# Performance work log

Measured on AMD Instinct MI355X. Metric: run time of the kernel, lower is better.

Reference implementation:

```python
import jax, jax.numpy as jnp
import numpy as np

SHAPE = (64, 64, 64)
N0 = 4000
K = 5  # subm conv kernel size -> 125 taps


def _neighbors(coors, shp):
    # coors: [N,4] int (b,z,y,x), batch=1. Returns [N,125] int32 neighbor row ids, -1 if absent.
    offs = np.stack(np.meshgrid(np.arange(-2, 3), np.arange(-2, 3), np.arange(-2, 3), indexing='ij'), -1).reshape(-1, 3)
    shp = np.asarray(shp)
    grid = -np.ones(tuple(shp), np.int32)
    grid[coors[:, 1], coors[:, 2], coors[:, 3]] = np.arange(len(coors), dtype=np.int32)
    nb = coors[:, None, 1:4] + offs[None]  # [N,125,3]
    valid = ((nb >= 0) & (nb < shp)).all(-1)
    nbc = np.clip(nb, 0, shp - 1)
    nbr = grid[nbc[..., 0], nbc[..., 1], nbc[..., 2]]
    return np.where(valid, nbr, -1).astype(np.int32)


def _pool_map(coors, shp):
    # kernel 2 stride 2 sparse max pool: parent cell = spatial // 2
    out_shp = [s // 2 for s in shp]
    sp = coors[:, 1:4] // 2
    lin = (sp[:, 0] * out_shp[1] + sp[:, 1]) * out_shp[2] + sp[:, 2]
    uniq, inv = np.unique(lin, return_inverse=True)
    z = uniq // (out_shp[1] * out_shp[2])
    r = uniq % (out_shp[1] * out_shp[2])
    nc = np.stack([np.zeros_like(z), z, r // out_shp[2], r % out_shp[2]], 1).astype(np.int32)
    return inv.astype(np.int32), nc, out_shp


_PAIRS = [(3, 64), (64, 64), (64, 96), (96, 96), (96, 128), (128, 128), (128, 160), (160, 160), (160, 192), (192, 192), (192, 224), (224, 224), (224, 256), (256, 256)]
_WNAMES = ['w0a', 'w0b', 'w1a', 'w1b', 'w2a', 'w2b', 'w3a', 'w3b', 'w4a', 'w4b', 'w5a', 'w5b', 'w6a', 'w6b']


def setup_inputs() -> dict:
    rng = np.random.RandomState(0)
    lin = rng.choice(SHAPE[0] * SHAPE[1] * SHAPE[2], N0, replace=False)
    z = lin // (SHAPE[1] * SHAPE[2])
    r = lin % (SHAPE[1] * SHAPE[2])
    coors = np.stack([np.zeros_like(z), z, r // SHAPE[2], r % SHAPE[2]], 1).astype(np.int32)
    inp = {}
    c, shp = coors, list(SHAPE)
    for l in range(7):
        inp['nbr%d' % l] = jnp.asarray(_neighbors(c, shp))
        if l < 6:
            pm, c, shp = _pool_map(c, shp)
            inp['pool%d' % l] = jnp.asarray(pm)
    key = jax.random.key(0)
    for name, (ci, co) in zip(_WNAMES, _PAIRS):
        key, k = jax.random.split(key)
        inp[name] = jax.random.normal(k, (K ** 3, ci, co), jnp.float32) * (K ** 3 * ci) ** -0.5
    key, kf = jax.random.split(key)
    inp['features'] = jax.random.normal(kf, (N0, 3), jnp.float32)
    inp['coors'] = jnp.asarray(coors)
    inp['batch_size'] = 1
    return inp


def _subm(feats, nbr, w):
    # gather-GEMM-scatter form of SubMConv3d (bias=False): out active set == in active set
    valid = nbr >= 0  # [N,125]
    g = jnp.take(feats, jnp.maximum(nbr, 0), axis=0)  # [N,125,Cin]
    g = jnp.where(valid[:, :, None], g, jnp.zeros((), feats.dtype))
    return jnp.einsum('nkc,kco->no', g, w)  # [N,Cout]


def reference(features, coors, batch_size, nbr0, nbr1, nbr2, nbr3, nbr4, nbr5, nbr6, pool0, pool1, pool2, pool3, pool4, pool5, w0a, w0b, w1a, w1b, w2a, w2b, w3a, w3b, w4a, w4b, w5a, w5b, w6a, w6b):
    nbrs = (nbr0, nbr1, nbr2, nbr3, nbr4, nbr5, nbr6)
    pools = (pool0, pool1, pool2, pool3, pool4, pool5)
    ws = ((w0a, w0b), (w1a, w1b), (w2a, w2b), (w3a, w3b), (w4a, w4b), (w5a, w5b), (w6a, w6b))
    x = features
    for l in range(7):
        x = _subm(x, nbrs[l], ws[l][0])
        x = _subm(x, nbrs[l], ws[l][1])
        if l < 6:
            # sparse max pool over active voxels of each 2x2x2 cell
            x = jax.ops.segment_max(x, pools[l], num_segments=nbrs[l + 1].shape[0])
    return x
```

## Files before the change

### kernel.cpp

```cpp
#include <hip/hip_runtime.h>
#include <stddef.h>
#include <stdint.h>

#define KTAPS 125

typedef _Float16 f16x8 __attribute__((ext_vector_type(8)));
typedef _Float16 f16x4 __attribute__((ext_vector_type(4)));
typedef float    f32x4 __attribute__((ext_vector_type(4)));

template<int NT>
__global__ __launch_bounds__(256) void subm_mfma(
    const _Float16* __restrict__ finh, const int* __restrict__ nbr,
    const _Float16* __restrict__ wt, _Float16* __restrict__ Pout,
    int N, int CinP, int TS)
{
    constexpr int BN = NT * 32;
    constexpr int DEPTH = (NT <= 5) ? 4 : 2;
    __shared__ int       nbs[16][64];
    __shared__ unsigned  msk[16][2];
    __shared__ unsigned char vtl[2][16];
    __shared__ int       vcs[2];
    __shared__ unsigned short sjc[2][128];

    const int tid  = threadIdx.x;
    const int lane = tid & 63;
    const int wid  = tid >> 6;
    const int wy   = wid & 1;
    const int wx   = wid >> 1;
    const int r15  = lane & 15;
    const int g4   = lane >> 4;
    const int row0 = blockIdx.x * 64;
    const int k0   = (blockIdx.y * KTAPS) / TS;
    const int k1   = ((blockIdx.y + 1) * KTAPS) / TS;
    const int KR   = k1 - k0;
    const int CC   = CinP >> 5;

    #pragma unroll
    for (int p = 0; p < 4; ++p) {
        int e = tid + p * 256;
        if (e < KR * 64) {
            int j = e >> 6, r = e & 63;
            int gr = row0 + r;
            nbs[j][r] = (gr < N) ? nbr[(size_t)gr * KTAPS + k0 + j] : -1;
        }
    }
    __syncthreads();
    for (int j = wid; j < KR; j += 4) {
        unsigned long long m = __ballot(nbs[j][lane] >= 0);
        if (lane == 0) { msk[j][0] = (unsigned)m; msk[j][1] = (unsigned)(m >> 32); }
    }
    __syncthreads();
    if (wid < 2) {
        int c = 0;
        for (int j = 0; j < KR; ++j)
            if (msk[j][wid]) { if (lane == 0) vtl[wid][c] = (unsigned char)j; ++c; }
        if (lane == 0) vcs[wid] = c;
        int TT = c * CC;
        for (int t = lane; t < TT; t += 64) {
            int j = vtl[wid][t / CC];
            int cc = t - (t / CC) * CC;
            sjc[wid][t] = (unsigned short)((j << 8) | cc);
        }
    }
    __syncthreads();
    const int T = vcs[wy] * CC;

    f32x4 acc[2][NT];
    #pragma unroll
    for (int mt = 0; mt < 2; ++mt)
        #pragma unroll
        for (int nf = 0; nf < NT; ++nf)
            acc[mt][nf] = (f32x4){0.f, 0.f, 0.f, 0.f};

    if (T > 0) {
        const size_t wchunk = (size_t)32 * BN;
        const int    boffh  = (g4 * BN + wx * (NT * 16) + r15) * 8;

        auto LOADA = [&](f16x8 (&a)[2], int j, int c) {
            unsigned mm = __builtin_amdgcn_readfirstlane(msk[j][wy]);
            if (mm & 0xFFFFu) {
                int src = nbs[j][wy * 32 + r15];
                if (src < 0) src = N;
                a[0] = *(const f16x8*)(finh + (size_t)src * CinP + c * 32 + g4 * 8);
            }
            if (mm >> 16) {
                int src = nbs[j][wy * 32 + 16 + r15];
                if (src < 0) src = N;
                a[1] = *(const f16x8*)(finh + (size_t)src * CinP + c * 32 + g4 * 8);
            }
        };
        auto LOADB = [&](f16x8 (&b)[NT], int j, int c) {
            const _Float16* base = wt + ((size_t)(k0 + j) * CC + c) * wchunk;
            #pragma unroll
            for (int nf = 0; nf < NT; ++nf)
                b[nf] = *(const f16x8*)&base[boffh + nf * 128];
        };
        auto LD = [&](f16x8 (&a)[2], f16x8 (&b)[NT], int t) {
            if (t < T) {
                int e = sjc[wy][t];
                int j = e >> 8, c = e & 255;
                LOADA(a, j, c); LOADB(b, j, c);
            }
        };
        auto CP = [&](f16x8 (&a)[2], f16x8 (&b)[NT], int t) {
            int j = sjc[wy][t] >> 8;
            unsigned mm = __builtin_amdgcn_readfirstlane(msk[j][wy]);
            if (mm & 0xFFFFu)
                #pragma unroll
                for (int nf = 0; nf < NT; ++nf)
                    acc[0][nf] = __builtin_amdgcn_mfma_f32_16x16x32_f16(a[0], b[nf], acc[0][nf], 0, 0, 0);
            if (mm >> 16)
                #pragma unroll
                for (int nf = 0; nf < NT; ++nf)
                    acc[1][nf] = __builtin_amdgcn_mfma_f32_16x16x32_f16(a[1], b[nf], acc[1][nf], 0, 0, 0);
        };

        if constexpr (DEPTH == 4) {
            f16x8 A0[2], B0[NT], A1[2], B1[NT], A2[2], B2[NT], A3[2], B3[NT];
            LD(A0, B0, 0); LD(A1, B1, 1); LD(A2, B2, 2); LD(A3, B3, 3);
            int t = 0;
            while (true) {
                CP(A0, B0, t); LD(A0, B0, t + 4); if (++t >= T) break;
                CP(A1, B1, t); LD(A1, B1, t + 4); if (++t >= T) break;
                CP(A2, B2, t); LD(A2, B2, t + 4); if (++t >= T) break;
                CP(A3, B3, t); LD(A3, B3, t + 4); if (++t >= T) break;
            }
        } else {
            f16x8 A0[2], B0[NT], A1[2], B1[NT];
            LD(A0, B0, 0); LD(A1, B1, 1);
            int t = 0;
            while (true) {
                CP(A0, B0, t); LD(A0, B0, t + 2); if (++t >= T) break;
                CP(A1, B1, t); LD(A1, B1, t + 2); if (++t >= T) break;
            }
        }
    }

    _Float16* base = Pout + (size_t)blockIdx.y * ((size_t)N * BN);
    #pragma unroll
    for (int mt = 0; mt < 2; ++mt) {
        #pragma unroll
        for (int q = 0; q < 4; ++q) {
            int r = row0 + wy * 32 + mt * 16 + g4 * 4 + q;
            if (r < N) {
                #pragma unroll
                for (int nf = 0; nf < NT; ++nf)
                    base[(size_t)r * BN + wx * (NT * 16) + nf * 16 + r15] =
                        (_Float16)acc[mt][nf][q];
            }
        }
    }
}

__global__ __launch_bounds__(256) void reduce_a(
    const _Float16* __restrict__ P, _Float16* __restrict__ H,
    int N, int BN, int S, float scale)
{
    int idx = blockIdx.x * 256 + threadIdx.x;
    size_t i4 = (size_t)idx * 4;
    if (i4 >= (size_t)(N + 1) * BN) return;
    f16x4 h;
    if (i4 >= (size_t)N * BN) {
        h[0] = h[1] = h[2] = h[3] = (_Float16)0.f;
    } else {
        float s0 = 0.f, s1 = 0.f, s2 = 0.f, s3 = 0.f;
        size_t stride = (size_t)N * BN;
        for (int si = 0; si < S; ++si) {
            f16x4 p = *(const f16x4*)&P[si * stride + i4];
            s0 += (float)p[0]; s1 += (float)p[1]; s2 += (float)p[2]; s3 += (float)p[3];
        }
        h[0] = (_Float16)(s0 * scale); h[1] = (_Float16)(s1 * scale);
        h[2] = (_Float16)(s2 * scale); h[3] = (_Float16)(s3 * scale);
    }
    *(f16x4*)&H[i4] = h;
}

__device__ __forceinline__ unsigned enc_f32(float f) {
    unsigned u = __float_as_uint(f);
    return (u & 0x80000000u) ? ~u : (u | 0x80000000u);
}

__global__ __launch_bounds__(256) void reduce_b(
    const _Float16* __restrict__ P, const int* __restrict__ pm,
    unsigned* __restrict__ ENC, float* __restrict__ dout,
    int N, int BN, int S, float fscale, int isLast)
{
    int idx = blockIdx.x * 256 + threadIdx.x;
    size_t i4 = (size_t)idx * 4;
    if (i4 >= (size_t)N * BN) return;
    float s0 = 0.f, s1 = 0.f, s2 = 0.f, s3 = 0.f;
    size_t stride = (size_t)N * BN;
    for (int si = 0; si < S; ++si) {
        f16x4 p = *(const f16x4*)&P[si * stride + i4];
        s0 += (float)p[0]; s1 += (float)p[1]; s2 += (float)p[2]; s3 += (float)p[3];
    }
    if (isLast) {
        dout[i4 + 0] = s0 * fscale; dout[i4 + 1] = s1 * fscale;
        dout[i4 + 2] = s2 * fscale; dout[i4 + 3] = s3 * fscale;
    } else {
        int row = (int)(i4 / BN), c = (int)(i4 % BN);
        unsigned* e = &ENC[(size_t)pm[row] * BN + c];
        atomicMax(e + 0, enc_f32(s0));
        atomicMax(e + 1, enc_f32(s1));
        atomicMax(e + 2, enc_f32(s2));
        atomicMax(e + 3, enc_f32(s3));
    }
}

__global__ __launch_bounds__(256) void pool_dec(
    unsigned* __restrict__ ENC, _Float16* __restrict__ H, int Nout, int C, float scale)
{
    int i = blockIdx.x * 256 + threadIdx.x;
    if (i < Nout * C) {
        unsigned u = ENC[i];
        float f = __uint_as_float((u & 0x80000000u) ? (u ^ 0x80000000u) : ~u);
        H[i] = (_Float16)(f * scale);
        ENC[i] = 0u;
    } else if (i < (Nout + 1) * C) {
        H[i] = (_Float16)0.f;
    }
}

__global__ __launch_bounds__(256) void tap_flags(
    const int* n0, const int* n1, const int* n2, const int* n3,
    const int* n4, const int* n5, const int* n6,
    int N0, int N1, int N2, int N3, int N4, int N5, int N6,
    unsigned* __restrict__ flags)
{
    int l = blockIdx.y, k = blockIdx.x;
    const int* nb; int N;
    switch (l) {
        case 0: nb = n0; N = N0; break;  case 1: nb = n1; N = N1; break;
        case 2: nb = n2; N = N2; break;  case 3: nb = n3; N = N3; break;
        case 4: nb = n4; N = N4; break;  case 5: nb = n5; N = N5; break;
        default: nb = n6; N = N6; break;
    }
    bool any = false;
    for (int r = threadIdx.x; r < N; r += 256) any |= (nb[(size_t)r * KTAPS + k] >= 0);
    bool a = __syncthreads_or(any);
    if (threadIdx.x == 0) flags[l * KTAPS + k] = a ? 1u : 0u;
}

__global__ __launch_bounds__(256) void cvt_weights(
    const float* __restrict__ wa, const float* __restrict__ wb,
    _Float16* __restrict__ ta, _Float16* __restrict__ tb,
    const unsigned* __restrict__ flags,
    int CinA, int CCa, int CoutA, int splitA,
    int CinB, int CCb, int CoutB)
{
    int k = blockIdx.x;
    if (!flags[k]) return;
    int by = blockIdx.y;
    const float* w; _Float16* t; int Cin, CC, Cout, cc, c0;
    if (by < splitA) { w = wa; t = ta; Cin = CinA; CC = CCa; Cout = CoutA;
                       cc = by / (CoutA / 32); c0 = (by % (CoutA / 32)) * 32; }
    else { by -= splitA; w = wb; t = tb; Cin = CinB; CC = CCb; Cout = CoutB;
           cc = by / (CoutB / 32); c0 = (by % (CoutB / 32)) * 32; }

    __shared__ float T[32][33];
    int tid = threadIdx.x;
    #pragma unroll
    for (int p = 0; p < 4; ++p) {
        int e = tid + p * 256;
        int r = e >> 5, cl = e & 31;
        int ci = cc * 32 + r;
        T[r][cl] = (ci < Cin) ? w[((size_t)k * Cin + ci) * Cout + c0 + cl] : 0.f;
    }
    __syncthreads();
    if (tid < 128) {
        int g = tid >> 5, co = tid & 31;
        f16x8 h;
        #pragma unroll
        for (int j = 0; j < 8; ++j) h[j] = (_Float16)T[g * 8 + j][co];
        *(f16x8*)&t[((size_t)k * CC + cc) * (32 * (size_t)Cout) + ((size_t)g * Cout + c0 + co) * 8] = h;
    }
}

__global__ __launch_bounds__(256) void init_all(
    const float* __restrict__ feat, _Float16* __restrict__ H,
    unsigned* __restrict__ ENC, int N0, int nE)
{
    int i = blockIdx.x * 256 + threadIdx.x;
    if (i < nE) ENC[i] = 0u;
    int nH = (N0 + 1) * 32;
    if (i < nH) {
        int r = i >> 5, cl = i & 31;
        H[i] = (r < N0 && cl < 3) ? (_Float16)feat[r * 3 + cl] : (_Float16)0.f;
    }
}

static inline int pick_ts(int rt)
{
    int ts = (1024 + rt - 1) / rt;
    if (ts < 8) ts = 8;
    if (ts > 42) ts = 42;
    return ts;
}

static void conv_dispatch(int NT, dim3 g, hipStream_t s, const _Float16* fin, const int* nbr,
                          const _Float16* wt, _Float16* P, int N, int CinP, int TS)
{
    switch (NT) {
        case 2: subm_mfma<2><<<g,256,0,s>>>(fin,nbr,wt,P,N,CinP,TS); break;
        case 3: subm_mfma<3><<<g,256,0,s>>>(fin,nbr,wt,P,N,CinP,TS); break;
        case 4: subm_mfma<4><<<g,256,0,s>>>(fin,nbr,wt,P,N,CinP,TS); break;
        case 5: subm_mfma<5><<<g,256,0,s>>>(fin,nbr,wt,P,N,CinP,TS); break;
        case 6: subm_mfma<6><<<g,256,0,s>>>(fin,nbr,wt,P,N,CinP,TS); break;
        case 7: subm_mfma<7><<<g,256,0,s>>>(fin,nbr,wt,P,N,CinP,TS); break;
        case 8: subm_mfma<8><<<g,256,0,s>>>(fin,nbr,wt,P,N,CinP,TS); break;
    }
}

extern "C" void kernel_launch(void* const* d_in, const int* in_sizes, int n_in,
                              void* d_out, int out_size, void* d_ws, size_t ws_size,
                              hipStream_t stream)
{
    const int* nbr[7]; const int* pm[6]; int Ns[7];
    {
        int idx = 0;
        for (int l = 0; l < 7; ++l) {
            nbr[l] = (const int*)d_in[idx];
            Ns[l]  = in_sizes[idx] / KTAPS;
            ++idx;
            if (l < 6) { pm[l] = (const int*)d_in[idx]; ++idx; }
        }
    }
    const float* w[14];
    for (int i = 0; i < 14; ++i) w[i] = (const float*)d_in[13 + i];
    const float* feat = (const float*)d_in[27];

    static const int CI[14]  = {3,64, 64,96, 96,128, 128,160, 160,192, 192,224, 224,256};
    static const int CO[14]  = {64,64, 96,96, 128,128, 160,160, 192,192, 224,224, 256,256};
    static const int KSH[14] = {0,3, 2,2, 1,1, 0,0, 0,1, 0,2, 2,3};
    const float finalScale = 1.0f / 131072.0f;
    int CinP[14];
    for (int i = 0; i < 14; ++i) CinP[i] = (CI[i] < 32) ? 32 : CI[i];

    int TSv[14];
    size_t maxP = 0, maxHa = 0, maxHb = 0, maxE = 0, maxWA = 0, maxWB = 0;
    for (int l = 0; l < 7; ++l) {
        int rt = (Ns[l] + 63) / 64;
        int ts = pick_ts(rt);
        TSv[2*l] = ts; TSv[2*l+1] = ts;
        size_t pa = (size_t)ts * Ns[l] * CO[2*l];   if (pa > maxP) maxP = pa;
        size_t pb = (size_t)ts * Ns[l] * CO[2*l+1]; if (pb > maxP) maxP = pb;
        size_t ha = (size_t)(Ns[l] + 1) * CinP[2*l];   if (ha > maxHa) maxHa = ha;
        size_t hb = (size_t)(Ns[l] + 1) * CinP[2*l+1]; if (hb > maxHb) maxHb = hb;
        if (l < 6) { size_t e = (size_t)Ns[l+1] * CO[2*l+1]; if (e > maxE) maxE = e; }
        size_t wa = (size_t)KTAPS * CinP[2*l] * CO[2*l];     if (wa > maxWA) maxWA = wa;
        size_t wb = (size_t)KTAPS * CinP[2*l+1] * CO[2*l+1]; if (wb > maxWB) maxWB = wb;
    }
    size_t off = 0;
    auto carve = [&](size_t bytes) -> void* {
        void* p = (char*)d_ws + off;
        off = (off + bytes + 255) & ~(size_t)255;
        return p;
    };
    _Float16*  P    = (_Float16*)carve(maxP * 2);
    _Float16*  Ha   = (_Float16*)carve(maxHa * 2);
    _Float16*  Hb   = (_Float16*)carve(maxHb * 2);
    unsigned*  ENC  = (unsigned*)carve(maxE * 4);
    _Float16*  wtA  = (_Float16*)carve(maxWA * 2);
    _Float16*  wtB  = (_Float16*)carve(maxWB * 2);
    unsigned*  flags= (unsigned*)carve(7 * KTAPS * 4);

    {
        int nMax = (int)maxE;
        int nH = (Ns[0] + 1) * 32;
        if (nH > nMax) nMax = nH;
        init_all<<<(nMax + 255) / 256, 256, 0, stream>>>(feat, Ha, ENC, Ns[0], (int)maxE);
    }
    tap_flags<<<dim3(KTAPS, 7), 256, 0, stream>>>(
        nbr[0], nbr[1], nbr[2], nbr[3], nbr[4], nbr[5], nbr[6],
        Ns[0], Ns[1], Ns[2], Ns[3], Ns[4], Ns[5], Ns[6], flags);

    for (int l = 0; l < 7; ++l) {
        int ia = 2 * l, ib = 2 * l + 1;
        int N = Ns[l];
        int rt = (N + 63) / 64;
        int splitA = (CinP[ia] / 32) * (CO[ia] / 32);
        int splitB = (CinP[ib] / 32) * (CO[ib] / 32);
        cvt_weights<<<dim3(KTAPS, splitA + splitB), 256, 0, stream>>>(
            w[ia], w[ib], wtA, wtB, flags + l * KTAPS,
            CI[ia], CinP[ia] / 32, CO[ia], splitA,
            CI[ib], CinP[ib] / 32, CO[ib]);

        {
            int TS = TSv[ia], BN = CO[ia];
            conv_dispatch(BN / 32, dim3(rt, TS), stream, Ha, nbr[l], wtA, P, N, CinP[ia], TS);
            int tot = ((N + 1) * BN + 3) / 4;
            reduce_a<<<(tot + 255) / 256, 256, 0, stream>>>(P, Hb, N, BN, TS,
                                                            (float)(1 << KSH[ib]));
        }
        {
            int TS = TSv[ib], BN = CO[ib];
            conv_dispatch(BN / 32, dim3(rt, TS), stream, Hb, nbr[l], wtB, P, N, CinP[ib], TS);
            int tot = (N * BN + 3) / 4;
            reduce_b<<<(tot + 255) / 256, 256, 0, stream>>>(
                P, (l < 6) ? pm[l] : nullptr, ENC, (float*)d_out,
                N, BN, TS, finalScale, (l == 6) ? 1 : 0);
        }
        if (l < 6) {
            int C = CO[ib], Nout = Ns[l + 1];
            int tot2 = (Nout + 1) * C;
            pool_dec<<<(tot2 + 255) / 256, 256, 0, stream>>>(ENC, Ha, Nout, C,
                                                             (float)(1 << KSH[2 * l + 2]));
        }
    }
}
```

Measured before the change: 484.7 us.

## Add channel-chunk split-K and swizzled 1D grid for subm conv kernels

Adds a channel-chunk split dimension (CS) so the single-row-tile deepest layer can spread work over 125 taps times channel chunks. Larger layers move to a 1D grid whose block index is swizzled into groups of 8 taps per row tile. The tap-split count is now rounded to a multiple of 8, with a cap of 56. The aim is more parallelism on the small late layers and better scheduling locality, at the cost of larger partial-sum buffers and more reduction work.

Result: slower. 1.604 ms (+230.9%).

```diff
diff --git a/kernel.cpp b/kernel.cpp
--- a/kernel.cpp
+++ b/kernel.cpp
@@ -12,7 +12,7 @@
 __global__ __launch_bounds__(256) void subm_mfma(
     const _Float16* __restrict__ finh, const int* __restrict__ nbr,
     const _Float16* __restrict__ wt, _Float16* __restrict__ Pout,
-    int N, int CinP, int TS)
+    int N, int CinP, int TS, int CS, int SWZ)
 {
     constexpr int BN = NT * 32;
     constexpr int DEPTH = (NT <= 5) ? 4 : 2;
@@ -29,11 +29,27 @@
     const int wx   = wid >> 1;
     const int r15  = lane & 15;
     const int g4   = lane >> 4;
-    const int row0 = blockIdx.x * 64;
-    const int k0   = (blockIdx.y * KTAPS) / TS;
-    const int k1   = ((blockIdx.y + 1) * KTAPS) / TS;
+
+    int rowtile, ts, cs;
+    if (SWZ) {
+        int L   = blockIdx.x;
+        int q   = L >> 3;
+        int TSo = TS >> 3;
+        ts      = (L & 7) + 8 * (q % TSo);
+        rowtile = q / TSo;
+        cs      = 0;
+    } else {
+        rowtile = blockIdx.x; ts = blockIdx.y; cs = blockIdx.z;
+    }
+
+    const int row0 = rowtile * 64;
+    const int k0   = (ts * KTAPS) / TS;
+    const int k1   = ((ts + 1) * KTAPS) / TS;
     const int KR   = k1 - k0;
     const int CC   = CinP >> 5;
+    const int cc0  = (cs * CC) / CS;
+    const int cc1  = ((cs + 1) * CC) / CS;
+    const int NC   = cc1 - cc0;
 
     #pragma unroll
     for (int p = 0; p < 4; ++p) {
@@ -55,15 +71,15 @@
         for (int j = 0; j < KR; ++j)
             if (msk[j][wid]) { if (lane == 0) vtl[wid][c] = (unsigned char)j; ++c; }
         if (lane == 0) vcs[wid] = c;
-        int TT = c * CC;
+        int TT = c * NC;
         for (int t = lane; t < TT; t += 64) {
-            int j = vtl[wid][t / CC];
-            int cc = t - (t / CC) * CC;
+            int j = vtl[wid][t / NC];
+            int cc = cc0 + (t - (t / NC) * NC);
             sjc[wid][t] = (unsigned short)((j << 8) | cc);
         }
     }
     __syncthreads();
-    const int T = vcs[wy] * CC;
+    const int T = vcs[wy] * NC;
 
     f32x4 acc[2][NT];
     #pragma unroll
@@ -136,7 +152,7 @@
         }
     }
 
-    _Float16* base = Pout + (size_t)blockIdx.y * ((size_t)N * BN);
+    _Float16* base = Pout + (size_t)(ts * CS + cs) * ((size_t)N * BN);
     #pragma unroll
     for (int mt = 0; mt < 2; ++mt) {
         #pragma unroll
@@ -289,25 +305,19 @@
     }
 }
 
-static inline int pick_ts(int rt)
-{
-    int ts = (1024 + rt - 1) / rt;
-    if (ts < 8) ts = 8;
-    if (ts > 42) ts = 42;
-    return ts;
-}
+static inline int round8(int x) { int r = ((x + 4) / 8) * 8; if (r < 8) r = 8; if (r > 56) r = 56; return r; }
 
 static void conv_dispatch(int NT, dim3 g, hipStream_t s, const _Float16* fin, const int* nbr,
-                          const _Float16* wt, _Float16* P, int N, int CinP, int TS)
+                          const _Float16* wt, _Float16* P, int N, int CinP, int TS, int CS, int SWZ)
 {
     switch (NT) {
-        case 2: subm_mfma<2><<<g,256,0,s>>>(fin,nbr,wt,P,N,CinP,TS); break;
-        case 3: subm_mfma<3><<<g,256,0,s>>>(fin,nbr,wt,P,N,CinP,TS); break;
-        case 4: subm_mfma<4><<<g,256,0,s>>>(fin,nbr,wt,P,N,CinP,TS); break;
-        case 5: subm_mfma<5><<<g,256,0,s>>>(fin,nbr,wt,P,N,CinP,TS); break;
-        case 6: subm_mfma<6><<<g,256,0,s>>>(fin,nbr,wt,P,N,CinP,TS); break;
-        case 7: subm_mfma<7><<<g,256,0,s>>>(fin,nbr,wt,P,N,CinP,TS); break;
-        case 8: subm_mfma<8><<<g,256,0,s>>>(fin,nbr,wt,P,N,CinP,TS); break;
+        case 2: subm_mfma<2><<<g,256,0,s>>>(fin,nbr,wt,P,N,CinP,TS,CS,SWZ); break;
+        case 3: subm_mfma<3><<<g,256,0,s>>>(fin,nbr,wt,P,N,CinP,TS,CS,SWZ); break;
+        case 4: subm_mfma<4><<<g,256,0,s>>>(fin,nbr,wt,P,N,CinP,TS,CS,SWZ); break;
+        case 5: subm_mfma<5><<<g,256,0,s>>>(fin,nbr,wt,P,N,CinP,TS,CS,SWZ); break;
+        case 6: subm_mfma<6><<<g,256,0,s>>>(fin,nbr,wt,P,N,CinP,TS,CS,SWZ); break;
+        case 7: subm_mfma<7><<<g,256,0,s>>>(fin,nbr,wt,P,N,CinP,TS,CS,SWZ); break;
+        case 8: subm_mfma<8><<<g,256,0,s>>>(fin,nbr,wt,P,N,CinP,TS,CS,SWZ); break;
     }
 }
 
@@ -336,14 +346,17 @@
     int CinP[14];
     for (int i = 0; i < 14; ++i) CinP[i] = (CI[i] < 32) ? 32 : CI[i];
 
-    int TSv[14];
+    int TSv[14], CSv[14], SWv[14];
     size_t maxP = 0, maxHa = 0, maxHb = 0, maxE = 0, maxWA = 0, maxWB = 0;
     for (int l = 0; l < 7; ++l) {
         int rt = (Ns[l] + 63) / 64;
-        int ts = pick_ts(rt);
-        TSv[2*l] = ts; TSv[2*l+1] = ts;
-        size_t pa = (size_t)ts * Ns[l] * CO[2*l];   if (pa > maxP) maxP = pa;
-        size_t pb = (size_t)ts * Ns[l] * CO[2*l+1]; if (pb > maxP) maxP = pb;
+        for (int q = 0; q < 2; ++q) {
+            int i = 2 * l + q;
+            if (rt > 1) { TSv[i] = round8(1024 / rt); CSv[i] = 1; SWv[i] = 1; }
+            else        { TSv[i] = KTAPS; CSv[i] = CinP[i] / 32; SWv[i] = 0; }
+            size_t p = (size_t)TSv[i] * CSv[i] * Ns[l] * CO[i];
+            if (p > maxP) maxP = p;
+        }
         size_t ha = (size_t)(Ns[l] + 1) * CinP[2*l];   if (ha > maxHa) maxHa = ha;
         size_t hb = (size_t)(Ns[l] + 1) * CinP[2*l+1]; if (hb > maxHb) maxHb = hb;
         if (l < 6) { size_t e = (size_t)Ns[l+1] * CO[2*l+1]; if (e > maxE) maxE = e; }
@@ -386,19 +399,21 @@
             CI[ib], CinP[ib] / 32, CO[ib]);
 
         {
-            int TS = TSv[ia], BN = CO[ia];
-            conv_dispatch(BN / 32, dim3(rt, TS), stream, Ha, nbr[l], wtA, P, N, CinP[ia], TS);
+            int TS = TSv[ia], CS = CSv[ia], BN = CO[ia];
+            dim3 g = SWv[ia] ? dim3(rt * TS) : dim3(rt, TS, CS);
+            conv_dispatch(BN / 32, g, stream, Ha, nbr[l], wtA, P, N, CinP[ia], TS, CS, SWv[ia]);
             int tot = ((N + 1) * BN + 3) / 4;
-            reduce_a<<<(tot + 255) / 256, 256, 0, stream>>>(P, Hb, N, BN, TS,
+            reduce_a<<<(tot + 255) / 256, 256, 0, stream>>>(P, Hb, N, BN, TS * CS,
                                                             (float)(1 << KSH[ib]));
         }
         {
-            int TS = TSv[ib], BN = CO[ib];
-            conv_dispatch(BN / 32, dim3(rt, TS), stream, Hb, nbr[l], wtB, P, N, CinP[ib], TS);
+            int TS = TSv[ib], CS = CSv[ib], BN = CO[ib];
+            dim3 g = SWv[ib] ? dim3(rt * TS) : dim3(rt, TS, CS);
+            conv_dispatch(BN / 32, g, stream, Hb, nbr[l], wtB, P, N, CinP[ib], TS, CS, SWv[ib]);
             int tot = (N * BN + 3) / 4;
             reduce_b<<<(tot + 255) / 256, 256, 0, stream>>>(
                 P, (l < 6) ? pm[l] : nullptr, ENC, (float*)d_out,
-                N, BN, TS, finalScale, (l == 6) ? 1 : 0);
+                N, BN, TS * CS, finalScale, (l == 6) ? 1 : 0);
         }
         if (l < 6) {
             int C = CO[ib], Nout = Ns[l + 1];
```
